# Kernel tuning notes

Measured on AMD Instinct MI355X. Metric: run time of the kernel, lower is better.

The kernel has to match this reference:

```python
import jax, jax.numpy as jnp
import numpy as np

INPUT, HIDDEN = 15, 20

def setup_inputs() -> dict:
    key = jax.random.key(0)
    k1, k2, k3, k4, k5 = jax.random.split(key, 5)
    B, T = 4096, 512
    s = 1.0 / np.sqrt(HIDDEN)  # torch default uniform init bound
    feature = jax.random.normal(k1, (B, T, INPUT), dtype=jnp.float32)
    W_ih = jax.random.uniform(k2, (HIDDEN, INPUT), jnp.float32, -s, s)
    W_hh = jax.random.uniform(k3, (HIDDEN, HIDDEN), jnp.float32, -s, s)
    b_ih = jax.random.uniform(k4, (HIDDEN,), jnp.float32, -s, s)
    b_hh = jax.random.uniform(k5, (HIDDEN,), jnp.float32, -s, s)
    return {"feature": feature, "W_ih": W_ih, "W_hh": W_hh, "b_ih": b_ih, "b_hh": b_hh}

def reference(feature, W_ih, W_hh, b_ih, b_hh):
    # h_t = tanh(x_t @ W_ih^T + b_ih + h_{t-1} @ W_hh^T + b_hh)
    B, T, _ = feature.shape
    # precompute input projections for all timesteps: [T, B, H]
    xp = jnp.einsum('bti,hi->tbh', feature, W_ih) + (b_ih + b_hh)
    h0 = jnp.zeros((B, HIDDEN), dtype=feature.dtype)
    def step(h, x_t):
        h_new = jnp.tanh(x_t + h @ W_hh.T)
        return h_new, None
    hn, _ = jax.lax.scan(step, h0, xp)
    return hn  # [B, H] == hn.squeeze() for num_layers=1
```

## Files before the change

### kernel.cpp

```cpp
#include <hip/hip_runtime.h>
#include <cstddef>


typedef float g4 __attribute__((ext_vector_type(4), aligned(4)));
typedef float g2 __attribute__((ext_vector_type(2), aligned(4)));
typedef float v4 __attribute__((ext_vector_type(4)));
typedef float f2 __attribute__((ext_vector_type(2)));

#define TT 512
#define IN 15
#define HD 20
#define CH 32
#define NCH (TT / CH)

__device__ __forceinline__ f2 lo2(v4 v) { return (f2){v.x, v.y}; }
__device__ __forceinline__ f2 hi2(v4 v) { return (f2){v.z, v.w}; }

__global__ __launch_bounds__(64) void rnn_fused(
    const float* __restrict__ feature, const float* __restrict__ W_ih,
    const float* __restrict__ W_hh, const float* __restrict__ b_ih,
    const float* __restrict__ b_hh, float* __restrict__ out, int B) {
  __shared__ float xb[2][3][CH][16];
  __shared__ float hl[4][HD];

  const int lane = threadIdx.x;
  const int g = lane / HD;
  const int j = lane - g * HD;
  const int gx = (g < 3) ? g : 2;
  const int bid = blockIdx.x;
  const int b = bid * 3 + g;

  for (int i = lane; i < 4 * HD; i += 64) ((float*)hl)[i] = 0.f;
  for (int i = lane; i < 2 * 3 * CH; i += 64) ((float*)xb)[i * 16 + 15] = 0.f;

  f2 wih[8];
  {
    const float* wr = W_ih + j * IN;
#pragma unroll
    for (int i = 0; i < 7; ++i) wih[i] = (f2){wr[2 * i], wr[2 * i + 1]};
    wih[7] = (f2){wr[14], 0.f};
  }
  f2 whh[10];
  {
    const float* wr = W_hh + j * HD;
#pragma unroll
    for (int i = 0; i < 10; ++i) whh[i] = (f2){wr[2 * i], wr[2 * i + 1]};
  }
  const float bias = b_ih[j] + b_hh[j];

  const int grA = lane >> 5;
  const int tcA = lane & 31;
  const int bc = B - 1;
  const int bA = min(bid * 3 + grA, bc);
  const int bB = min(bid * 3 + 2, bc);
  const float* baseA = feature + ((size_t)bA * TT + tcA) * IN;
  const float* baseB = feature + ((size_t)bB * TT + tcA) * IN;

  g4 rA0, rA1, rA2; g2 rA3; float rA4;
  g4 rB0, rB1, rB2; g2 rB3; float rB4;

  auto issue = [&](int t0) {
    const float* s = baseA + (size_t)t0 * IN;
    rA0 = *(const g4*)(s);      rA1 = *(const g4*)(s + 4);
    rA2 = *(const g4*)(s + 8);  rA3 = *(const g2*)(s + 12);
    rA4 = s[14];
    if (lane < 32) {
      const float* s2 = baseB + (size_t)t0 * IN;
      rB0 = *(const g4*)(s2);     rB1 = *(const g4*)(s2 + 4);
      rB2 = *(const g4*)(s2 + 8); rB3 = *(const g2*)(s2 + 12);
      rB4 = s2[14];
    }
  };
  auto commit = [&](int bsel) {
    float* d = &xb[bsel][grA][tcA][0];
    *(v4*)d = (v4)rA0; *(v4*)(d + 4) = (v4)rA1; *(v4*)(d + 8) = (v4)rA2;
    *(f2*)(d + 12) = (f2)rA3; d[14] = rA4;
    if (lane < 32) {
      float* d2 = &xb[bsel][2][tcA][0];
      *(v4*)d2 = (v4)rB0; *(v4*)(d2 + 4) = (v4)rB1; *(v4*)(d2 + 8) = (v4)rB2;
      *(f2*)(d2 + 12) = (f2)rB3; d2[14] = rB4;
    }
  };

  issue(0);
  commit(0);

  float hn = 0.f;
  const float* hrow = &hl[g][0];
  float* hwr = &hl[g][j];
  for (int c = 0; c < NCH; ++c) {
    if (c + 1 < NCH) issue((c + 1) * CH);
    const float* xrow = &xb[c & 1][gx][0][0];
#pragma unroll 4
    for (int tc = 0; tc < CH; ++tc) {
      const v4* xp = (const v4*)(xrow + tc * 16);
      v4 x0 = xp[0], x1 = xp[1], x2 = xp[2], x3 = xp[3];
      const v4* hp = (const v4*)hrow;
      v4 h0 = hp[0], h1 = hp[1], h2 = hp[2], h3 = hp[3], h4 = hp[4];
      f2 a0 = (f2){bias, 0.f}, a1 = (f2){0.f, 0.f};
      f2 a2 = (f2){0.f, 0.f},  a3 = (f2){0.f, 0.f};
      a0 += lo2(x0) * wih[0]; a1 += hi2(x0) * wih[1];
      a2 += lo2(x1) * wih[2]; a3 += hi2(x1) * wih[3];
      a0 += lo2(x2) * wih[4]; a1 += hi2(x2) * wih[5];
      a2 += lo2(x3) * wih[6]; a3 += hi2(x3) * wih[7];
      a0 += lo2(h0) * whh[0]; a1 += hi2(h0) * whh[1];
      a2 += lo2(h1) * whh[2]; a3 += hi2(h1) * whh[3];
      a0 += lo2(h2) * whh[4]; a1 += hi2(h2) * whh[5];
      a2 += lo2(h3) * whh[6]; a3 += hi2(h3) * whh[7];
      a0 += lo2(h4) * whh[8]; a1 += hi2(h4) * whh[9];
      f2 sv = (a0 + a1) + (a2 + a3);
      float s = sv.x + sv.y;
      float e = exp2f(s * 2.8853900817779268f);
      hn = 1.f - 2.f * __builtin_amdgcn_rcpf(1.f + e);
      *hwr = hn;
    }
    if (c + 1 < NCH) commit((c + 1) & 1);
  }
  if (g < 3 && b < B) out[(size_t)b * HD + j] = hn;
}

extern "C" void kernel_launch(void* const* d_in, const int* in_sizes, int n_in,
                              void* d_out, int out_size, void* d_ws, size_t ws_size,
                              hipStream_t stream) {
  const float* feature = (const float*)d_in[0];
  const float* W_ih    = (const float*)d_in[1];
  const float* W_hh    = (const float*)d_in[2];
  const float* b_ih    = (const float*)d_in[3];
  const float* b_hh    = (const float*)d_in[4];
  float* out = (float*)d_out;
  const int B = in_sizes[0] / (TT * IN);
  const int grid = (B + 2) / 3;
  rnn_fused<<<grid, 64, 0, stream>>>(feature, W_ih, W_hh, b_ih, b_hh, out, B);
}
```

Before: 241.7 us.

## Switch RNN recurrence to fp16 storage with fdot2 accumulation

Inputs and hidden state are stored in shared memory as fp16, and weights are packed as half2, so each step uses v_dot2_f32_f16 (fdot2) instead of packed fp32 FMAs. This halves LDS traffic per timestep and roughly halves the multiply-add instruction count on the serial dependency chain. Row padding of the x groups is changed to reduce bank conflicts. The cost is reduced precision: the hidden state is rounded to fp16 every step and errors can accumulate over 512 timesteps, which risks exceeding the tolerance.

Measured after the change: 233.6 us. 1.03x faster.

```diff
diff --git a/kernel.cpp b/kernel.cpp
--- a/kernel.cpp
+++ b/kernel.cpp
@@ -4,24 +4,29 @@
 
 typedef float g4 __attribute__((ext_vector_type(4), aligned(4)));
 typedef float g2 __attribute__((ext_vector_type(2), aligned(4)));
-typedef float v4 __attribute__((ext_vector_type(4)));
-typedef float f2 __attribute__((ext_vector_type(2)));
+typedef _Float16 h2  __attribute__((ext_vector_type(2)));
+typedef _Float16 v8h __attribute__((ext_vector_type(8)));
+typedef _Float16 v4h __attribute__((ext_vector_type(4)));
 
 #define TT 512
 #define IN 15
 #define HD 20
 #define CH 32
 #define NCH (TT / CH)
+#define XROW 16
+#define XGRP (CH * XROW + 16)
+#define XBUF (3 * XGRP)
+#define HROW 24
 
-__device__ __forceinline__ f2 lo2(v4 v) { return (f2){v.x, v.y}; }
-__device__ __forceinline__ f2 hi2(v4 v) { return (f2){v.z, v.w}; }
+#define P2(v, i) __builtin_shufflevector(v, v, 2 * (i), 2 * (i) + 1)
+#define FD(acc, p, w) acc = __builtin_amdgcn_fdot2(p, w, acc, false)
 
 __global__ __launch_bounds__(64) void rnn_fused(
     const float* __restrict__ feature, const float* __restrict__ W_ih,
     const float* __restrict__ W_hh, const float* __restrict__ b_ih,
     const float* __restrict__ b_hh, float* __restrict__ out, int B) {
-  __shared__ float xb[2][3][CH][16];
-  __shared__ float hl[4][HD];
+  __shared__ __align__(16) _Float16 xh[2 * XBUF];
+  __shared__ __align__(16) _Float16 hh[4 * HROW];
 
   const int lane = threadIdx.x;
   const int g = lane / HD;
@@ -30,21 +35,22 @@
   const int bid = blockIdx.x;
   const int b = bid * 3 + g;
 
-  for (int i = lane; i < 4 * HD; i += 64) ((float*)hl)[i] = 0.f;
-  for (int i = lane; i < 2 * 3 * CH; i += 64) ((float*)xb)[i * 16 + 15] = 0.f;
+  if (lane < 48) ((float*)hh)[lane] = 0.f;
 
-  f2 wih[8];
+  h2 wih[8];
   {
     const float* wr = W_ih + j * IN;
 #pragma unroll
-    for (int i = 0; i < 7; ++i) wih[i] = (f2){wr[2 * i], wr[2 * i + 1]};
-    wih[7] = (f2){wr[14], 0.f};
+    for (int i = 0; i < 7; ++i)
+      wih[i] = (h2){(_Float16)wr[2 * i], (_Float16)wr[2 * i + 1]};
+    wih[7] = (h2){(_Float16)wr[14], (_Float16)0.f};
   }
-  f2 whh[10];
+  h2 whh[10];
   {
     const float* wr = W_hh + j * HD;
 #pragma unroll
-    for (int i = 0; i < 10; ++i) whh[i] = (f2){wr[2 * i], wr[2 * i + 1]};
+    for (int i = 0; i < 10; ++i)
+      whh[i] = (h2){(_Float16)wr[2 * i], (_Float16)wr[2 * i + 1]};
   }
   const float bias = b_ih[j] + b_hh[j];
 
@@ -72,13 +78,19 @@
     }
   };
   auto commit = [&](int bsel) {
-    float* d = &xb[bsel][grA][tcA][0];
-    *(v4*)d = (v4)rA0; *(v4*)(d + 4) = (v4)rA1; *(v4*)(d + 8) = (v4)rA2;
-    *(f2*)(d + 12) = (f2)rA3; d[14] = rA4;
+    v8h lo = {(_Float16)rA0.x, (_Float16)rA0.y, (_Float16)rA0.z, (_Float16)rA0.w,
+              (_Float16)rA1.x, (_Float16)rA1.y, (_Float16)rA1.z, (_Float16)rA1.w};
+    v8h hi = {(_Float16)rA2.x, (_Float16)rA2.y, (_Float16)rA2.z, (_Float16)rA2.w,
+              (_Float16)rA3.x, (_Float16)rA3.y, (_Float16)rA4,   (_Float16)0.f};
+    _Float16* d = xh + bsel * XBUF + grA * XGRP + tcA * XROW;
+    *(v8h*)d = lo; *((v8h*)d + 1) = hi;
     if (lane < 32) {
-      float* d2 = &xb[bsel][2][tcA][0];
-      *(v4*)d2 = (v4)rB0; *(v4*)(d2 + 4) = (v4)rB1; *(v4*)(d2 + 8) = (v4)rB2;
-      *(f2*)(d2 + 12) = (f2)rB3; d2[14] = rB4;
+      v8h lo2 = {(_Float16)rB0.x, (_Float16)rB0.y, (_Float16)rB0.z, (_Float16)rB0.w,
+                 (_Float16)rB1.x, (_Float16)rB1.y, (_Float16)rB1.z, (_Float16)rB1.w};
+      v8h hi2 = {(_Float16)rB2.x, (_Float16)rB2.y, (_Float16)rB2.z, (_Float16)rB2.w,
+                 (_Float16)rB3.x, (_Float16)rB3.y, (_Float16)rB4,   (_Float16)0.f};
+      _Float16* d2 = xh + bsel * XBUF + 2 * XGRP + tcA * XROW;
+      *(v8h*)d2 = lo2; *((v8h*)d2 + 1) = hi2;
     }
   };
 
@@ -86,33 +98,32 @@
   commit(0);
 
   float hn = 0.f;
-  const float* hrow = &hl[g][0];
-  float* hwr = &hl[g][j];
+  const _Float16* hrd = hh + g * HROW;
+  _Float16* hwr = hh + g * HROW + j;
   for (int c = 0; c < NCH; ++c) {
     if (c + 1 < NCH) issue((c + 1) * CH);
-    const float* xrow = &xb[c & 1][gx][0][0];
+    const _Float16* xg = xh + (c & 1) * XBUF + gx * XGRP;
 #pragma unroll 4
     for (int tc = 0; tc < CH; ++tc) {
-      const v4* xp = (const v4*)(xrow + tc * 16);
-      v4 x0 = xp[0], x1 = xp[1], x2 = xp[2], x3 = xp[3];
-      const v4* hp = (const v4*)hrow;
-      v4 h0 = hp[0], h1 = hp[1], h2 = hp[2], h3 = hp[3], h4 = hp[4];
-      f2 a0 = (f2){bias, 0.f}, a1 = (f2){0.f, 0.f};
-      f2 a2 = (f2){0.f, 0.f},  a3 = (f2){0.f, 0.f};
-      a0 += lo2(x0) * wih[0]; a1 += hi2(x0) * wih[1];
-      a2 += lo2(x1) * wih[2]; a3 += hi2(x1) * wih[3];
-      a0 += lo2(x2) * wih[4]; a1 += hi2(x2) * wih[5];
-      a2 += lo2(x3) * wih[6]; a3 += hi2(x3) * wih[7];
-      a0 += lo2(h0) * whh[0]; a1 += hi2(h0) * whh[1];
-      a2 += lo2(h1) * whh[2]; a3 += hi2(h1) * whh[3];
-      a0 += lo2(h2) * whh[4]; a1 += hi2(h2) * whh[5];
-      a2 += lo2(h3) * whh[6]; a3 += hi2(h3) * whh[7];
-      a0 += lo2(h4) * whh[8]; a1 += hi2(h4) * whh[9];
-      f2 sv = (a0 + a1) + (a2 + a3);
-      float s = sv.x + sv.y;
+      v8h ha = *(const v8h*)hrd;
+      v8h hb = *(const v8h*)(hrd + 8);
+      v4h hc = *(const v4h*)(hrd + 16);
+      const v8h* xp = (const v8h*)(xg + tc * XROW);
+      v8h xa = xp[0], xb = xp[1];
+      float a0 = bias, a1 = 0.f, a2 = 0.f, a3 = 0.f;
+      FD(a0, P2(xa, 0), wih[0]); FD(a1, P2(xa, 1), wih[1]);
+      FD(a2, P2(xa, 2), wih[2]); FD(a3, P2(xa, 3), wih[3]);
+      FD(a0, P2(xb, 0), wih[4]); FD(a1, P2(xb, 1), wih[5]);
+      FD(a2, P2(xb, 2), wih[6]); FD(a3, P2(xb, 3), wih[7]);
+      FD(a0, P2(ha, 0), whh[0]); FD(a1, P2(ha, 1), whh[1]);
+      FD(a2, P2(ha, 2), whh[2]); FD(a3, P2(ha, 3), whh[3]);
+      FD(a0, P2(hb, 0), whh[4]); FD(a1, P2(hb, 1), whh[5]);
+      FD(a2, P2(hb, 2), whh[6]); FD(a3, P2(hb, 3), whh[7]);
+      FD(a0, P2(hc, 0), whh[8]); FD(a1, P2(hc, 1), whh[9]);
+      float s = (a0 + a1) + (a2 + a3);
       float e = exp2f(s * 2.8853900817779268f);
       hn = 1.f - 2.f * __builtin_amdgcn_rcpf(1.f + e);
-      *hwr = hn;
+      *hwr = (_Float16)hn;
     }
     if (c + 1 < NCH) commit((c + 1) & 1);
   }
```
